# Optimization experiments

Hardware: AMD Instinct MI355X
Metric: run time of the kernel (lower is better)

## Reference

```python
import jax, jax.numpy as jnp
import numpy as np

NQ = 4  # qubits
silu = jax.nn.silu


def _ry(t):
    c, s = jnp.cos(t / 2), jnp.sin(t / 2)
    return jnp.stack([jnp.stack([c, -s]), jnp.stack([s, c])]).astype(jnp.complex64)


def _rz(t):
    e = jnp.exp(-0.5j * t.astype(jnp.complex64))
    z = jnp.zeros((), jnp.complex64)
    return jnp.stack([jnp.stack([e, z]), jnp.stack([z, jnp.conj(e)])])


def _ap1(state, U, w):
    # apply 2x2 unitary U on wire w of a (2,)*NQ statevector
    s = jnp.tensordot(U, jnp.moveaxis(state, w, 0), axes=1)
    return jnp.moveaxis(s, 0, w)


def _cnot(state, c, t):
    s = jnp.moveaxis(state, (c, t), (0, 1))
    s = jnp.stack([s[0], s[1, ::-1]], axis=0)
    return jnp.moveaxis(s, (0, 1), (c, t))


def _circuit(inp, w):
    # batched 4-qubit state-vector simulation of the PennyLane qnode
    state = jnp.zeros((2,) * NQ, jnp.complex64).at[(0,) * NQ].set(1.0)
    for i in range(NQ):
        state = _ap1(state, _ry(inp[i]), i)
    for i in range(NQ):
        state = _ap1(state, _rz(w[i, 0]), i)
        state = _ap1(state, _ry(w[i, 1]), i)
    for i in range(NQ - 1):
        state = _cnot(state, i, i + 1)
    for i in range(NQ):
        state = _ap1(state, _rz(w[i + NQ, 0]), i)
        state = _ap1(state, _ry(w[i + NQ, 1]), i)
    p = state.real ** 2 + state.imag ** 2
    sign = jnp.array([1.0, -1.0], p.dtype)
    return jnp.stack([jnp.tensordot(p, sign, axes=[[i], [0]]).sum() for i in range(NQ)])


def _bn(x, p, eps=1e-5):
    # p: [4, C] = (gamma, beta, running_mean, running_var); eval-mode batchnorm
    g, b, m, v = p
    shp = (1, -1) + (1,) * (x.ndim - 2)
    return (x - m.reshape(shp)) * (g.reshape(shp) / jnp.sqrt(v.reshape(shp) + eps)) + b.reshape(shp)


def _conv(x, w, b, pad, dil=1):
    y = jax.lax.conv_general_dilated(x, w, (1,), [(pad, pad)], rhs_dilation=(dil,),
                                     dimension_numbers=('NCH', 'OIH', 'NCH'))
    return y + b[None, :, None]


def _forward(x, W1, b1, bn1, Wa1, ba1, bna1, Wa2, ba2, bna2,
             Wd1, bd1, bnd1, Wd2, bd2, bnd2, Wr1, br1, bnr1, Wr2, br2, bnr2,
             Wfm, bfm, qw, Wf1, bf1, bnf1, Wf2, bf2, bnf2, Wf3, bf3):
    h = silu(_bn(_conv(x, W1, b1, 2), bn1))                    # [B,64,L]
    a = silu(_bn(_conv(h, Wa1, ba1, 3), bna1))                 # [B,32,L]
    a = jax.nn.sigmoid(_bn(_conv(a, Wa2, ba2, 3), bna2))       # [B,64,L]
    h = h * a
    h = silu(_bn(_conv(h, Wd1, bd1, 2, 2), bnd1))              # [B,128,L]
    h = silu(_bn(_conv(h, Wd2, bd2, 4, 4), bnd2))              # [B,128,L]
    idn = h
    r = silu(_bn(_conv(h, Wr1, br1, 1), bnr1))
    r = _bn(_conv(r, Wr2, br2, 1), bnr2)                       # (dropout is identity in eval)
    h = silu(r + idn)
    g = h.mean(axis=2)                                         # global avg pool -> [B,128]
    qin = g @ Wfm.T + bfm                                      # feature map -> [B,4]
    q = jax.vmap(_circuit, in_axes=(0, None))(qin, qw)         # [B,4]
    x1 = silu(_bn(q @ Wf1.T + bf1, bnf1))
    x2 = silu(_bn(x1 @ Wf2.T + bf2, bnf2))
    return x2 @ Wf3.T + bf3                                    # [B,1]


def setup_inputs() -> dict:
    key = jax.random.key(0)
    ks = iter(jax.random.split(key, 64))

    def w(*shape, scale=0.05):
        return jax.random.normal(next(ks), shape, jnp.float32) * scale

    def bnp(c):
        g = 1.0 + 0.1 * jax.random.normal(next(ks), (c,), jnp.float32)
        b = 0.1 * jax.random.normal(next(ks), (c,), jnp.float32)
        m = 0.1 * jax.random.normal(next(ks), (c,), jnp.float32)
        v = 1.0 + 0.1 * jax.random.uniform(next(ks), (c,), jnp.float32)
        return jnp.stack([g, b, m, v])

    B, L = 128, 4096
    return dict(
        x=jax.random.normal(next(ks), (B, 1, L), jnp.float32),
        W1=w(64, 1, 5), b1=w(64), bn1=bnp(64),
        Wa1=w(32, 64, 7), ba1=w(32), bna1=bnp(32),
        Wa2=w(64, 32, 7), ba2=w(64), bna2=bnp(64),
        Wd1=w(128, 64, 3), bd1=w(128), bnd1=bnp(128),
        Wd2=w(128, 128, 3), bd2=w(128), bnd2=bnp(128),
        Wr1=w(128, 128, 3), br1=w(128), bnr1=bnp(128),
        Wr2=w(128, 128, 3), br2=w(128), bnr2=bnp(128),
        Wfm=w(4, 128), bfm=w(4),
        qw=jax.random.uniform(next(ks), (8, 2), jnp.float32, 0.0, 2 * np.pi),
        Wf1=w(64, 4, scale=0.2), bf1=w(64), bnf1=bnp(64),
        Wf2=w(32, 64, scale=0.2), bf2=w(32), bnf2=bnp(32),
        Wf3=w(1, 32, scale=0.2), bf3=w(1),
    )


def reference(x, W1, b1, bn1, Wa1, ba1, bna1, Wa2, ba2, bna2,
              Wd1, bd1, bnd1, Wd2, bd2, bnd2, Wr1, br1, bnr1, Wr2, br2, bnr2,
              Wfm, bfm, qw, Wf1, bf1, bnf1, Wf2, bf2, bnf2, Wf3, bf3):
    return _forward(x, W1, b1, bn1, Wa1, ba1, bna1, Wa2, ba2, bna2,
                    Wd1, bd1, bnd1, Wd2, bd2, bnd2, Wr1, br1, bnr1, Wr2, br2, bnr2,
                    Wfm, bfm, qw, Wf1, bf1, bnf1, Wf2, bf2, bnf2, Wf3, bf3)
```

## Files before the change

kernel.cpp:

```cpp
#include <hip/hip_runtime.h>
#include <math.h>

#define L_LEN 4096
#define DEV __device__ __forceinline__

typedef __attribute__((ext_vector_type(8))) _Float16 f16x8;
typedef __attribute__((ext_vector_type(4))) float   f32x4;

DEV float fexp_f(float x) { return exp2f(1.44269504f * x); }
DEV float silu_f(float x) { return x * __builtin_amdgcn_rcpf(1.f + fexp_f(-x)); }
DEV float sigm_f(float x) { return __builtin_amdgcn_rcpf(1.f + fexp_f(-x)); }

DEV void gload16(const void* g, void* l) {
    __builtin_amdgcn_global_load_lds(
        (const __attribute__((address_space(1))) void*)g,
        (__attribute__((address_space(3))) void*)l, 16, 0, 0);
}

__global__ __launch_bounds__(256) void conv1_k(
    const float* __restrict__ x, const float* __restrict__ W,
    const float* __restrict__ bias, const float* __restrict__ bnp,
    _Float16* __restrict__ out)
{
    __shared__ float sw[64 * 5];
    __shared__ float ssc[64], ssh[64];
    const int tid = threadIdx.x;
    if (tid < 64) {
        float g = bnp[tid], be = bnp[64 + tid], mn = bnp[128 + tid], vr = bnp[192 + tid];
        float sc = g * rsqrtf(vr + 1e-5f);
        ssc[tid] = sc;
        ssh[tid] = fmaf(bias[tid] - mn, sc, be);
    }
    for (int i = tid; i < 320; i += 256) sw[i] = W[i];
    __syncthreads();

    const int b = blockIdx.y;
    const int l = blockIdx.x * 64 + (tid >> 2);
    const int cq = (tid & 3) * 16;

    float win[5];
#pragma unroll
    for (int k = 0; k < 5; ++k) {
        int ix = l + k - 2;
        win[k] = (ix >= 0 && ix < L_LEN) ? x[(size_t)b * L_LEN + ix] : 0.f;
    }
    __align__(16) _Float16 vv[16];
#pragma unroll
    for (int j = 0; j < 16; ++j) {
        const int co = cq + j;
        float z = 0.f;
#pragma unroll
        for (int k = 0; k < 5; ++k) z = fmaf(sw[co * 5 + k], win[k], z);
        z = fmaf(z, ssc[co], ssh[co]);
        vv[j] = (_Float16)silu_f(z);
    }
    const size_t o = ((size_t)b * L_LEN + l) * 64 + cq;
    *(int4*)(out + o)     = *(const int4*)(vv);
    *(int4*)(out + o + 8) = *(const int4*)(vv + 8);
}

struct PrepArgs {
    const float* W[6];
    _Float16*    wf[6];
    int cin[6], cout[6], kk[6];
    int cum[7];
};

__global__ void prep_all_k(PrepArgs a)
{
    const int id0 = blockIdx.x * 256 + threadIdx.x;
    if (id0 >= a.cum[6]) return;
    int sg = 0;
    while (sg < 5 && id0 >= a.cum[sg + 1]) ++sg;
    const int id   = id0 - a.cum[sg];
    const int CIN  = a.cin[sg], COUT = a.cout[sg], K = a.kk[sg];
    const int NTILE = COUT / 16;
    const int lane = id & 63;
    int r = id >> 6;
    const int n = r % NTILE; r /= NTILE;
    const int t = r % K;
    const int s = r / K;

    const int co  = n * 16 + (lane & 15);
    const int cib = s * 32 + (lane >> 4) * 8;
    const float* W = a.W[sg];
    __align__(16) _Float16 v8[8];
#pragma unroll
    for (int j = 0; j < 8; ++j)
        v8[j] = (_Float16)W[((size_t)co * CIN + cib + j) * K + t];
    *(int4*)(a.wf[sg] + (size_t)id * 8) = *(const int4*)v8;
}

template <int CIN, int COUT, int K, int DIL, int MODE>
__launch_bounds__(256, 2) __global__ void conv_mfma_k(
    const _Float16* __restrict__ in, const _Float16* __restrict__ wf,
    const float* __restrict__ bias,  const float* __restrict__ bnp,
    const _Float16* __restrict__ aux, _Float16* __restrict__ out,
    float* __restrict__ gsum, const float* __restrict__ zpage)
{
    constexpr int SL    = CIN / 32;
    constexpr int P     = SL * K;
    constexpr int PADR  = ((K - 1) / 2) * DIL;
    constexpr int LWIN  = 128 + (K - 1) * DIL;
    constexpr int NT    = COUT / 32;
    constexpr int NTILE = COUT / 16;
    constexpr int SLOTS = CIN / 8 + 1;
    constexpr int RSTR  = SLOTS * 16;
    constexpr int CH_IN = LWIN * SLOTS;
    constexpr int STGB  = LWIN * RSTR;
    constexpr int ESTR  = COUT + 4;
    constexpr int EPIB  = 128 * ESTR * 2;
    constexpr int SMEMB = (MODE == 3) ? STGB : ((STGB > EPIB) ? STGB : EPIB);

    __shared__ __align__(16) char smem[SMEMB];
    __shared__ float pf[(MODE == 3) ? 2 : 1][COUT];

    const int tid   = threadIdx.x;
    const int lane  = tid & 63;
    const int w     = tid >> 6;
    const int wl    = w >> 1;
    const int wc    = w & 1;
    const int b     = blockIdx.z;
    const int l0    = blockIdx.x * 128;
    const int lan15 = lane & 15;
    const int kgB   = (lane >> 4) * 16;

    const size_t bL = (size_t)b * L_LEN;

    auto loadB = [&](int p, f16x8 (&dst)[NT]) {
        const _Float16* bbase = wf + (size_t)p * (NTILE * 512);
#pragma unroll
        for (int nt = 0; nt < NT; ++nt) {
            const int ntg = wc * NT + nt;
            dst[nt] = *(const f16x8*)(bbase + ntg * 512 + lane * 8);
        }
    };

    f32x4 acc[4][NT];
#pragma unroll
    for (int mt = 0; mt < 4; ++mt)
#pragma unroll
        for (int nt = 0; nt < NT; ++nt) acc[mt][nt] = (f32x4){0.f, 0.f, 0.f, 0.f};

    f16x8 brbuf[2][NT];

    for (int c = tid; c < CH_IN; c += 256) {
        const int row  = c / SLOTS;
        const int slot = c - row * SLOTS;
        const int gl   = l0 - PADR + row;
        const bool ok  = (slot < SLOTS - 1) & (gl >= 0) & (gl < L_LEN);
        const _Float16* s0 = in + ((bL + gl) * CIN + slot * 8);
        const void* src = ok ? (const void*)s0 : (const void*)zpage;
        gload16(src, smem + (size_t)c * 16);
    }
    loadB(0, brbuf[0]);
    if (P > 1) loadB(1, brbuf[1]);
    asm volatile("s_waitcnt vmcnt(0)" ::: "memory");
    __builtin_amdgcn_sched_barrier(0);
    __syncthreads();

#pragma unroll
    for (int pp = 0; pp < P; ++pp) {
        const int ss = pp / K;
        const int tt = pp % K;
#pragma unroll
        for (int mt = 0; mt < 4; ++mt) {
            const int row = wl * 64 + mt * 16 + lan15 + tt * DIL;
            const f16x8 a = *(const f16x8*)(smem + row * RSTR + ss * 64 + kgB);
#pragma unroll
            for (int nt = 0; nt < NT; ++nt) {
                acc[mt][nt] = __builtin_amdgcn_mfma_f32_16x16x32_f16(brbuf[pp & 1][nt], a, acc[mt][nt], 0, 0, 0);
            }
        }
        if (pp + 2 < P) loadB(pp + 2, brbuf[pp & 1]);
    }

    if constexpr (MODE == 3) {
#pragma unroll
        for (int nt = 0; nt < NT; ++nt) {
            const int co0 = (wc * NT + nt) * 16 + (lane >> 4) * 4;
            const float4 g4 = *(const float4*)&bnp[co0];
            const float4 b4 = *(const float4*)&bnp[COUT + co0];
            const float4 m4 = *(const float4*)&bnp[2 * COUT + co0];
            const float4 v4 = *(const float4*)&bnp[3 * COUT + co0];
            const float4 bi = *(const float4*)&bias[co0];
            float sc[4], sh[4];
            sc[0] = g4.x * rsqrtf(v4.x + 1e-5f); sh[0] = fmaf(bi.x - m4.x, sc[0], b4.x);
            sc[1] = g4.y * rsqrtf(v4.y + 1e-5f); sh[1] = fmaf(bi.y - m4.y, sc[1], b4.y);
            sc[2] = g4.z * rsqrtf(v4.z + 1e-5f); sh[2] = fmaf(bi.z - m4.z, sc[2], b4.z);
            sc[3] = g4.w * rsqrtf(v4.w + 1e-5f); sh[3] = fmaf(bi.w - m4.w, sc[3], b4.w);

            float ps[4] = {0.f, 0.f, 0.f, 0.f};
#pragma unroll
            for (int mt = 0; mt < 4; ++mt) {
                const int l = wl * 64 + mt * 16 + lan15;
                const size_t gi = (bL + l0 + l) * COUT + co0;
                _Float16 a4[4];
                *(int2*)a4 = *(const int2*)(aux + gi);
#pragma unroll
                for (int r = 0; r < 4; ++r)
                    ps[r] += silu_f(fmaf(acc[mt][nt][r], sc[r], sh[r]) + (float)a4[r]);
            }
#pragma unroll
            for (int r = 0; r < 4; ++r) {
                ps[r] += __shfl_xor(ps[r], 1, 64);
                ps[r] += __shfl_xor(ps[r], 2, 64);
                ps[r] += __shfl_xor(ps[r], 4, 64);
                ps[r] += __shfl_xor(ps[r], 8, 64);
            }
            if (lan15 == 0) {
#pragma unroll
                for (int r = 0; r < 4; ++r)
                    pf[wl][co0 + r] = ps[r];
            }
        }
        __syncthreads();
        if (tid < COUT)
            atomicAdd(&gsum[b * COUT + tid], pf[0][tid] + pf[1][tid]);
    } else {
        __syncthreads();
        _Float16* zl = (_Float16*)smem;
#pragma unroll
        for (int nt = 0; nt < NT; ++nt) {
            const int co0 = (wc * NT + nt) * 16 + (lane >> 4) * 4;
            const float4 g4 = *(const float4*)&bnp[co0];
            const float4 b4 = *(const float4*)&bnp[COUT + co0];
            const float4 m4 = *(const float4*)&bnp[2 * COUT + co0];
            const float4 v4 = *(const float4*)&bnp[3 * COUT + co0];
            const float4 bi = *(const float4*)&bias[co0];
            float sc[4], sh[4];
            sc[0] = g4.x * rsqrtf(v4.x + 1e-5f); sh[0] = fmaf(bi.x - m4.x, sc[0], b4.x);
            sc[1] = g4.y * rsqrtf(v4.y + 1e-5f); sh[1] = fmaf(bi.y - m4.y, sc[1], b4.y);
            sc[2] = g4.z * rsqrtf(v4.z + 1e-5f); sh[2] = fmaf(bi.z - m4.z, sc[2], b4.z);
            sc[3] = g4.w * rsqrtf(v4.w + 1e-5f); sh[3] = fmaf(bi.w - m4.w, sc[3], b4.w);
#pragma unroll
            for (int mt = 0; mt < 4; ++mt) {
                const int l_loc = wl * 64 + mt * 16 + lan15;
                __align__(8) _Float16 h4[4];
#pragma unroll
                for (int r = 0; r < 4; ++r)
                    h4[r] = (_Float16)fmaf(acc[mt][nt][r], sc[r], sh[r]);
                *(int2*)&zl[l_loc * ESTR + co0] = *(const int2*)h4;
            }
        }
        __syncthreads();

        constexpr int CO8 = COUT / 8;
        constexpr int LG  = (CO8 == 16) ? 4 : (CO8 == 8) ? 3 : 2;
        constexpr int RPI = 64 / CO8;
        const int co = (lane & (CO8 - 1)) * 8;

#pragma unroll
        for (int s2 = 0; s2 < CO8 / 2; ++s2) {
            const int l = w * 32 + s2 * RPI + (lane >> LG);
            _Float16 z8[8];
            *(int4*)z8 = *(const int4*)&zl[l * ESTR + co];
            const size_t gidx = (bL + l0 + l) * COUT + co;
            __align__(16) _Float16 o8[8];
            if constexpr (MODE == 0) {
#pragma unroll
                for (int j = 0; j < 8; ++j) o8[j] = (_Float16)silu_f((float)z8[j]);
            } else {
                _Float16 g8[8];
                *(int4*)g8 = *(const int4*)(aux + gidx);
#pragma unroll
                for (int j = 0; j < 8; ++j) o8[j] = (_Float16)((float)g8[j] * sigm_f((float)z8[j]));
            }
            *(int4*)(out + gidx) = *(const int4*)o8;
        }
    }
}

template <int BW> DEV void g_ry(float (&re)[16], float (&im)[16], float t) {
    float s, c; sincosf(0.5f * t, &s, &c);
#pragma unroll
    for (int i = 0; i < 16; ++i)
        if (!(i & BW)) {
            const int j = i | BW;
            float r0 = re[i], q0 = im[i], r1 = re[j], q1 = im[j];
            re[i] = c * r0 - s * r1; im[i] = c * q0 - s * q1;
            re[j] = s * r0 + c * r1; im[j] = s * q0 + c * q1;
        }
}
template <int BW> DEV void g_rz(float (&re)[16], float (&im)[16], float t) {
    float s, c; sincosf(0.5f * t, &s, &c);
#pragma unroll
    for (int i = 0; i < 16; ++i) {
        float r = re[i], q = im[i];
        if (i & BW) { re[i] = r * c - q * s; im[i] = q * c + r * s; }
        else        { re[i] = r * c + q * s; im[i] = q * c - r * s; }
    }
}
template <int BC, int BT> DEV void g_cnot(float (&re)[16], float (&im)[16]) {
#pragma unroll
    for (int i = 0; i < 16; ++i)
        if ((i & BC) && !(i & BT)) {
            const int j = i | BT;
            float r = re[i]; re[i] = re[j]; re[j] = r;
            float q = im[i]; im[i] = im[j]; im[j] = q;
        }
}

__global__ __launch_bounds__(64) void qhead_k(
    const float* __restrict__ gsum, const float* __restrict__ Wfm,
    const float* __restrict__ bfm, const float* __restrict__ qw,
    const float* __restrict__ Wf1, const float* __restrict__ bf1, const float* __restrict__ bnf1,
    const float* __restrict__ Wf2, const float* __restrict__ bf2, const float* __restrict__ bnf2,
    const float* __restrict__ Wf3, const float* __restrict__ bf3,
    float* __restrict__ out)
{
    const int b = blockIdx.x, t = threadIdx.x;
    const float inv = 1.f / (float)L_LEN;

    float part[4];
    {
        const float gv0 = gsum[b * 128 + t] * inv;
        const float gv1 = gsum[b * 128 + 64 + t] * inv;
#pragma unroll
        for (int j = 0; j < 4; ++j)
            part[j] = gv0 * Wfm[j * 128 + t] + gv1 * Wfm[j * 128 + 64 + t];
    }
#pragma unroll
    for (int j = 0; j < 4; ++j) {
#pragma unroll
        for (int m = 1; m < 64; m <<= 1)
            part[j] += __shfl_xor(part[j], m, 64);
        part[j] += bfm[j];
    }

    float re[16], im[16];
#pragma unroll
    for (int i = 0; i < 16; ++i) { re[i] = 0.f; im[i] = 0.f; }
    re[0] = 1.f;
    g_ry<8>(re, im, part[0]); g_ry<4>(re, im, part[1]); g_ry<2>(re, im, part[2]); g_ry<1>(re, im, part[3]);
    g_rz<8>(re, im, qw[0]);  g_ry<8>(re, im, qw[1]);
    g_rz<4>(re, im, qw[2]);  g_ry<4>(re, im, qw[3]);
    g_rz<2>(re, im, qw[4]);  g_ry<2>(re, im, qw[5]);
    g_rz<1>(re, im, qw[6]);  g_ry<1>(re, im, qw[7]);
    g_cnot<8, 4>(re, im); g_cnot<4, 2>(re, im); g_cnot<2, 1>(re, im);
    g_rz<8>(re, im, qw[8]);  g_ry<8>(re, im, qw[9]);
    g_rz<4>(re, im, qw[10]); g_ry<4>(re, im, qw[11]);
    g_rz<2>(re, im, qw[12]); g_ry<2>(re, im, qw[13]);
    g_rz<1>(re, im, qw[14]); g_ry<1>(re, im, qw[15]);

    float pr[16];
#pragma unroll
    for (int i = 0; i < 16; ++i) pr[i] = re[i] * re[i] + im[i] * im[i];
    float q[4];
#pragma unroll
    for (int w = 0; w < 4; ++w) {
        const int bw = 8 >> w;
        float e = 0.f;
#pragma unroll
        for (int i = 0; i < 16; ++i) e += (i & bw) ? -pr[i] : pr[i];
        q[w] = e;
    }

    __shared__ float x1[64], x2[32];
    {
        float a = bf1[t];
#pragma unroll
        for (int k = 0; k < 4; ++k) a = fmaf(q[k], Wf1[t * 4 + k], a);
        const float sc = bnf1[t] / sqrtf(bnf1[192 + t] + 1e-5f);
        const float z  = (a - bnf1[128 + t]) * sc + bnf1[64 + t];
        x1[t] = silu_f(z);
    }
    __syncthreads();
    if (t < 32) {
        float a = bf2[t];
        for (int k = 0; k < 64; ++k) a = fmaf(x1[k], Wf2[t * 64 + k], a);
        const float sc = bnf2[t] / sqrtf(bnf2[96 + t] + 1e-5f);
        const float z  = (a - bnf2[64 + t]) * sc + bnf2[32 + t];
        x2[t] = silu_f(z);
    }
    __syncthreads();
    if (t == 0) {
        float a = bf3[0];
        for (int k = 0; k < 32; ++k) a = fmaf(x2[k], Wf3[k], a);
        out[b] = a;
    }
}

extern "C" void kernel_launch(void* const* d_in, const int* in_sizes, int n_in,
                              void* d_out, int out_size, void* d_ws, size_t ws_size,
                              hipStream_t stream)
{
    (void)n_in; (void)out_size;
    const float* x    = (const float*)d_in[0];
    const float* W1   = (const float*)d_in[1];
    const float* b1   = (const float*)d_in[2];
    const float* bn1  = (const float*)d_in[3];
    const float* Wa1  = (const float*)d_in[4];
    const float* ba1  = (const float*)d_in[5];
    const float* bna1 = (const float*)d_in[6];
    const float* Wa2  = (const float*)d_in[7];
    const float* ba2  = (const float*)d_in[8];
    const float* bna2 = (const float*)d_in[9];
    const float* Wd1  = (const float*)d_in[10];
    const float* bdd1 = (const float*)d_in[11];
    const float* bnd1 = (const float*)d_in[12];
    const float* Wd2  = (const float*)d_in[13];
    const float* bdd2 = (const float*)d_in[14];
    const float* bnd2 = (const float*)d_in[15];
    const float* Wr1  = (const float*)d_in[16];
    const float* br1  = (const float*)d_in[17];
    const float* bnr1 = (const float*)d_in[18];
    const float* Wr2  = (const float*)d_in[19];
    const float* br2  = (const float*)d_in[20];
    const float* bnr2 = (const float*)d_in[21];
    const float* Wfm  = (const float*)d_in[22];
    const float* bfm  = (const float*)d_in[23];
    const float* qw   = (const float*)d_in[24];
    const float* Wf1  = (const float*)d_in[25];
    const float* bf1  = (const float*)d_in[26];
    const float* bnf1 = (const float*)d_in[27];
    const float* Wf2  = (const float*)d_in[28];
    const float* bf2  = (const float*)d_in[29];
    const float* bnf2 = (const float*)d_in[30];
    const float* Wf3  = (const float*)d_in[31];
    const float* bf3  = (const float*)d_in[32];

    const int B = in_sizes[0] / L_LEN;

    char* base = (char*)d_ws;
    size_t off = 0;
    auto alloc = [&](size_t bytes) -> char* {
        off = (off + 255) & ~(size_t)255;
        char* p = base + off;
        off += bytes;
        return p;
    };

    float* gbuf  = (float*)alloc((size_t)B * 128 * 4);
    float* zpage = (float*)alloc(256);

    auto wfrag = [&](int cin, int cout, int k) -> _Float16* {
        return (_Float16*)alloc((size_t)k * cout * cin * 2);
    };
    _Float16* wa1f = wfrag(64, 32, 7);
    _Float16* wa2f = wfrag(32, 64, 7);
    _Float16* wd1f = wfrag(64, 128, 3);
    _Float16* wd2f = wfrag(128, 128, 3);
    _Float16* wr1f = wfrag(128, 128, 3);
    _Float16* wr2f = wfrag(128, 128, 3);

    const size_t fixed = (off + 255) & ~(size_t)255;
    const size_t PS = (size_t)2 * L_LEN * 256;
    size_t avail = (ws_size > fixed + 4096) ? ws_size - fixed - 4096 : 0;
    int chunk = B;
    while (chunk > 1 && (size_t)chunk * PS > avail) chunk >>= 1;

    auto aplane = [&](int C, int c) -> _Float16* {
        return (_Float16*)alloc((size_t)c * L_LEN * C * 2);
    };
    _Float16* h0 = aplane(64,  chunk);
    _Float16* a1 = aplane(32,  chunk);
    (void)     aplane(32,  chunk);
    _Float16* d1 = aplane(128, chunk);
    _Float16* d2 = h0;
    _Float16* r1 = d1;

    PrepArgs pa;
    pa.W[0] = Wa1; pa.wf[0] = wa1f; pa.cin[0] = 64;  pa.cout[0] = 32;  pa.kk[0] = 7;
    pa.W[1] = Wa2; pa.wf[1] = wa2f; pa.cin[1] = 32;  pa.cout[1] = 64;  pa.kk[1] = 7;
    pa.W[2] = Wd1; pa.wf[2] = wd1f; pa.cin[2] = 64;  pa.cout[2] = 128; pa.kk[2] = 3;
    pa.W[3] = Wd2; pa.wf[3] = wd2f; pa.cin[3] = 128; pa.cout[3] = 128; pa.kk[3] = 3;
    pa.W[4] = Wr1; pa.wf[4] = wr1f; pa.cin[4] = 128; pa.cout[4] = 128; pa.kk[4] = 3;
    pa.W[5] = Wr2; pa.wf[5] = wr2f; pa.cin[5] = 128; pa.cout[5] = 128; pa.kk[5] = 3;
    pa.cum[0] = 0;
    for (int i = 0; i < 6; ++i)
        pa.cum[i + 1] = pa.cum[i] + (pa.cin[i] / 32) * pa.kk[i] * (pa.cout[i] / 16) * 64;
    prep_all_k<<<dim3((pa.cum[6] + 255) / 256), dim3(256), 0, stream>>>(pa);

    hipMemsetAsync(gbuf, 0, (size_t)B * 128 * sizeof(float), stream);
    hipMemsetAsync(zpage, 0, 256, stream);

    const dim3 blk(256);
    for (int sft = 0; sft < B; sft += chunk) {
        const int c = (chunk < B - sft) ? chunk : (B - sft);
        const dim3 cg(L_LEN / 128, 1, c);
        conv1_k<<<dim3(64, c), blk, 0, stream>>>(x + (size_t)sft * L_LEN, W1, b1, bn1, h0);
        conv_mfma_k<64, 32, 7, 1, 0><<<cg, blk, 0, stream>>>(h0, wa1f, ba1, bna1, nullptr, a1, nullptr, zpage);
        conv_mfma_k<32, 64, 7, 1, 1><<<cg, blk, 0, stream>>>(a1, wa2f, ba2, bna2, h0, h0, nullptr, zpage);
        conv_mfma_k<64, 128, 3, 2, 0><<<cg, blk, 0, stream>>>(h0, wd1f, bdd1, bnd1, nullptr, d1, nullptr, zpage);
        conv_mfma_k<128, 128, 3, 4, 0><<<cg, blk, 0, stream>>>(d1, wd2f, bdd2, bnd2, nullptr, d2, nullptr, zpage);
        conv_mfma_k<128, 128, 3, 1, 0><<<cg, blk, 0, stream>>>(d2, wr1f, br1, bnr1, nullptr, r1, nullptr, zpage);
        conv_mfma_k<128, 128, 3, 1, 3><<<cg, blk, 0, stream>>>(r1, wr2f, br2, bnr2, d2, nullptr, gbuf + (size_t)sft * 128, zpage);
    }

    qhead_k<<<dim3(B), dim3(64), 0, stream>>>(gbuf, Wfm, bfm, qw,
                                              Wf1, bf1, bnf1, Wf2, bf2, bnf2, Wf3, bf3,
                                              (float*)d_out);
}
```

Measured before the change: 454.1 us.

## Process two L-tiles per block with double-buffered input staging

```diff
diff --git a/kernel.cpp b/kernel.cpp
--- a/kernel.cpp
+++ b/kernel.cpp
@@ -98,6 +98,7 @@
     const _Float16* __restrict__ aux, _Float16* __restrict__ out,
     float* __restrict__ gsum, const float* __restrict__ zpage)
 {
+    constexpr int TT    = 2;
     constexpr int SL    = CIN / 32;
     constexpr int P     = SL * K;
     constexpr int PADR  = ((K - 1) / 2) * DIL;
@@ -107,10 +108,12 @@
     constexpr int SLOTS = CIN / 8 + 1;
     constexpr int RSTR  = SLOTS * 16;
     constexpr int CH_IN = LWIN * SLOTS;
-    constexpr int STGB  = LWIN * RSTR;
+    constexpr int BUFB  = LWIN * RSTR;
     constexpr int ESTR  = COUT + 4;
     constexpr int EPIB  = 128 * ESTR * 2;
-    constexpr int SMEMB = (MODE == 3) ? STGB : ((STGB > EPIB) ? STGB : EPIB);
+    constexpr bool EFIT = (EPIB <= BUFB);
+    constexpr int SMEMB = (MODE == 3) ? 2 * BUFB
+                        : (EFIT ? 2 * BUFB : 2 * BUFB + EPIB);
 
     __shared__ __align__(16) char smem[SMEMB];
     __shared__ float pf[(MODE == 3) ? 2 : 1][COUT];
@@ -121,11 +124,24 @@
     const int wl    = w >> 1;
     const int wc    = w & 1;
     const int b     = blockIdx.z;
-    const int l0    = blockIdx.x * 128;
     const int lan15 = lane & 15;
     const int kgB   = (lane >> 4) * 16;
+    const int tile0 = blockIdx.x * TT;
 
     const size_t bL = (size_t)b * L_LEN;
+
+    auto stage_in = [&](int l0s, int buf) {
+        char* dst = smem + buf * BUFB;
+        for (int c = tid; c < CH_IN; c += 256) {
+            const int row  = c / SLOTS;
+            const int slot = c - row * SLOTS;
+            const int gl   = l0s - PADR + row;
+            const bool ok  = (slot < SLOTS - 1) & (gl >= 0) & (gl < L_LEN);
+            const _Float16* s0 = in + ((bL + gl) * CIN + slot * 8);
+            const void* src = ok ? (const void*)s0 : (const void*)zpage;
+            gload16(src, dst + (size_t)c * 16);
+        }
+    };
 
     auto loadB = [&](int p, f16x8 (&dst)[NT]) {
         const _Float16* bbase = wf + (size_t)p * (NTILE * 512);
@@ -136,137 +152,154 @@
         }
     };
 
-    f32x4 acc[4][NT];
-#pragma unroll
-    for (int mt = 0; mt < 4; ++mt)
-#pragma unroll
-        for (int nt = 0; nt < NT; ++nt) acc[mt][nt] = (f32x4){0.f, 0.f, 0.f, 0.f};
-
-    f16x8 brbuf[2][NT];
-
-    for (int c = tid; c < CH_IN; c += 256) {
-        const int row  = c / SLOTS;
-        const int slot = c - row * SLOTS;
-        const int gl   = l0 - PADR + row;
-        const bool ok  = (slot < SLOTS - 1) & (gl >= 0) & (gl < L_LEN);
-        const _Float16* s0 = in + ((bL + gl) * CIN + slot * 8);
-        const void* src = ok ? (const void*)s0 : (const void*)zpage;
-        gload16(src, smem + (size_t)c * 16);
-    }
-    loadB(0, brbuf[0]);
-    if (P > 1) loadB(1, brbuf[1]);
-    asm volatile("s_waitcnt vmcnt(0)" ::: "memory");
-    __builtin_amdgcn_sched_barrier(0);
-    __syncthreads();
-
-#pragma unroll
-    for (int pp = 0; pp < P; ++pp) {
-        const int ss = pp / K;
-        const int tt = pp % K;
-#pragma unroll
-        for (int mt = 0; mt < 4; ++mt) {
-            const int row = wl * 64 + mt * 16 + lan15 + tt * DIL;
-            const f16x8 a = *(const f16x8*)(smem + row * RSTR + ss * 64 + kgB);
+    stage_in(tile0 * 128, 0);
+
+#pragma unroll
+    for (int ti = 0; ti < TT; ++ti) {
+        const int l0  = (tile0 + ti) * 128;
+        char* curb = smem + (ti & 1) * BUFB;
+
+        asm volatile("s_waitcnt vmcnt(0)" ::: "memory");
+        __builtin_amdgcn_sched_barrier(0);
+        __syncthreads();
+
+        f32x4 acc[4][NT];
+#pragma unroll
+        for (int mt = 0; mt < 4; ++mt)
+#pragma unroll
+            for (int nt = 0; nt < NT; ++nt) acc[mt][nt] = (f32x4){0.f, 0.f, 0.f, 0.f};
+
+        f16x8 brbuf[2][NT];
+        loadB(0, brbuf[0]);
+        if (P > 1) loadB(1, brbuf[1]);
+
+#pragma unroll
+        for (int pp = 0; pp < P; ++pp) {
+            const int ss = pp / K;
+            const int tt = pp % K;
+#pragma unroll
+            for (int mt = 0; mt < 4; ++mt) {
+                const int row = wl * 64 + mt * 16 + lan15 + tt * DIL;
+                const f16x8 a = *(const f16x8*)(curb + row * RSTR + ss * 64 + kgB);
+#pragma unroll
+                for (int nt = 0; nt < NT; ++nt)
+                    acc[mt][nt] = __builtin_amdgcn_mfma_f32_16x16x32_f16(brbuf[pp & 1][nt], a, acc[mt][nt], 0, 0, 0);
+            }
+            if (pp + 2 < P) loadB(pp + 2, brbuf[pp & 1]);
+        }
+
+        if constexpr (MODE == 3) {
+            int2 a16[4][NT];
+#pragma unroll
+            for (int mt = 0; mt < 4; ++mt)
+#pragma unroll
+                for (int nt = 0; nt < NT; ++nt) {
+                    const int co0 = (wc * NT + nt) * 16 + (lane >> 4) * 4;
+                    const int l = wl * 64 + mt * 16 + lan15;
+                    a16[mt][nt] = *(const int2*)(aux + (bL + l0 + l) * COUT + co0);
+                }
+            if (ti + 1 < TT) stage_in(l0 + 128, (ti + 1) & 1);
+
 #pragma unroll
             for (int nt = 0; nt < NT; ++nt) {
-                acc[mt][nt] = __builtin_amdgcn_mfma_f32_16x16x32_f16(brbuf[pp & 1][nt], a, acc[mt][nt], 0, 0, 0);
+                const int co0 = (wc * NT + nt) * 16 + (lane >> 4) * 4;
+                const float4 g4 = *(const float4*)&bnp[co0];
+                const float4 b4 = *(const float4*)&bnp[COUT + co0];
+                const float4 m4 = *(const float4*)&bnp[2 * COUT + co0];
+                const float4 v4 = *(const float4*)&bnp[3 * COUT + co0];
+                const float4 bi = *(const float4*)&bias[co0];
+                float sc[4], sh[4];
+                sc[0] = g4.x * rsqrtf(v4.x + 1e-5f); sh[0] = fmaf(bi.x - m4.x, sc[0], b4.x);
+                sc[1] = g4.y * rsqrtf(v4.y + 1e-5f); sh[1] = fmaf(bi.y - m4.y, sc[1], b4.y);
+                sc[2] = g4.z * rsqrtf(v4.z + 1e-5f); sh[2] = fmaf(bi.z - m4.z, sc[2], b4.z);
+                sc[3] = g4.w * rsqrtf(v4.w + 1e-5f); sh[3] = fmaf(bi.w - m4.w, sc[3], b4.w);
+
+                float ps[4] = {0.f, 0.f, 0.f, 0.f};
+#pragma unroll
+                for (int mt = 0; mt < 4; ++mt) {
+                    _Float16 a4[4];
+                    *(int2*)a4 = a16[mt][nt];
+#pragma unroll
+                    for (int r = 0; r < 4; ++r)
+                        ps[r] += silu_f(fmaf(acc[mt][nt][r], sc[r], sh[r]) + (float)a4[r]);
+                }
+#pragma unroll
+                for (int r = 0; r < 4; ++r) {
+                    ps[r] += __shfl_xor(ps[r], 1, 64);
+                    ps[r] += __shfl_xor(ps[r], 2, 64);
+                    ps[r] += __shfl_xor(ps[r], 4, 64);
+                    ps[r] += __shfl_xor(ps[r], 8, 64);
+                }
+                if (lan15 == 0) {
+#pragma unroll
+                    for (int r = 0; r < 4; ++r)
+                        pf[wl][co0 + r] = ps[r];
+                }
             }
-        }
-        if (pp + 2 < P) loadB(pp + 2, brbuf[pp & 1]);
-    }
-
-    if constexpr (MODE == 3) {
-#pragma unroll
-        for (int nt = 0; nt < NT; ++nt) {
-            const int co0 = (wc * NT + nt) * 16 + (lane >> 4) * 4;
-            const float4 g4 = *(const float4*)&bnp[co0];
-            const float4 b4 = *(const float4*)&bnp[COUT + co0];
-            const float4 m4 = *(const float4*)&bnp[2 * COUT + co0];
-            const float4 v4 = *(const float4*)&bnp[3 * COUT + co0];
-            const float4 bi = *(const float4*)&bias[co0];
-            float sc[4], sh[4];
-            sc[0] = g4.x * rsqrtf(v4.x + 1e-5f); sh[0] = fmaf(bi.x - m4.x, sc[0], b4.x);
-            sc[1] = g4.y * rsqrtf(v4.y + 1e-5f); sh[1] = fmaf(bi.y - m4.y, sc[1], b4.y);
-            sc[2] = g4.z * rsqrtf(v4.z + 1e-5f); sh[2] = fmaf(bi.z - m4.z, sc[2], b4.z);
-            sc[3] = g4.w * rsqrtf(v4.w + 1e-5f); sh[3] = fmaf(bi.w - m4.w, sc[3], b4.w);
-
-            float ps[4] = {0.f, 0.f, 0.f, 0.f};
-#pragma unroll
-            for (int mt = 0; mt < 4; ++mt) {
-                const int l = wl * 64 + mt * 16 + lan15;
-                const size_t gi = (bL + l0 + l) * COUT + co0;
-                _Float16 a4[4];
-                *(int2*)a4 = *(const int2*)(aux + gi);
-#pragma unroll
-                for (int r = 0; r < 4; ++r)
-                    ps[r] += silu_f(fmaf(acc[mt][nt][r], sc[r], sh[r]) + (float)a4[r]);
+            __syncthreads();
+            if (tid < COUT)
+                atomicAdd(&gsum[b * COUT + tid], pf[0][tid] + pf[1][tid]);
+        } else {
+            constexpr int CO8 = COUT / 8;
+            constexpr int LG  = (CO8 == 16) ? 4 : (CO8 == 8) ? 3 : 2;
+            constexpr int RPI = 64 / CO8;
+            const int cos = (lane & (CO8 - 1)) * 8;
+
+            int4 gx[CO8 / 2];
+            if constexpr (MODE == 1) {
+#pragma unroll
+                for (int s2 = 0; s2 < CO8 / 2; ++s2) {
+                    const int l = w * 32 + s2 * RPI + (lane >> LG);
+                    gx[s2] = *(const int4*)(aux + (bL + l0 + l) * COUT + cos);
+                }
             }
-#pragma unroll
-            for (int r = 0; r < 4; ++r) {
-                ps[r] += __shfl_xor(ps[r], 1, 64);
-                ps[r] += __shfl_xor(ps[r], 2, 64);
-                ps[r] += __shfl_xor(ps[r], 4, 64);
-                ps[r] += __shfl_xor(ps[r], 8, 64);
+            if (ti + 1 < TT) stage_in(l0 + 128, (ti + 1) & 1);
+
+            __syncthreads();
+            _Float16* zl = EFIT ? (_Float16*)curb : (_Float16*)(smem + 2 * BUFB);
+#pragma unroll
+            for (int nt = 0; nt < NT; ++nt) {
+                const int co0 = (wc * NT + nt) * 16 + (lane >> 4) * 4;
+                const float4 g4 = *(const float4*)&bnp[co0];
+                const float4 b4 = *(const float4*)&bnp[COUT + co0];
+                const float4 m4 = *(const float4*)&bnp[2 * COUT + co0];
+                const float4 v4 = *(const float4*)&bnp[3 * COUT + co0];
+                const float4 bi = *(const float4*)&bias[co0];
+                float sc[4], sh[4];
+                sc[0] = g4.x * rsqrtf(v4.x + 1e-5f); sh[0] = fmaf(bi.x - m4.x, sc[0], b4.x);
+                sc[1] = g4.y * rsqrtf(v4.y + 1e-5f); sh[1] = fmaf(bi.y - m4.y, sc[1], b4.y);
+                sc[2] = g4.z * rsqrtf(v4.z + 1e-5f); sh[2] = fmaf(bi.z - m4.z, sc[2], b4.z);
+                sc[3] = g4.w * rsqrtf(v4.w + 1e-5f); sh[3] = fmaf(bi.w - m4.w, sc[3], b4.w);
+#pragma unroll
+                for (int mt = 0; mt < 4; ++mt) {
+                    const int l_loc = wl * 64 + mt * 16 + lan15;
+                    __align__(8) _Float16 h4[4];
+#pragma unroll
+                    for (int r = 0; r < 4; ++r)
+                        h4[r] = (_Float16)fmaf(acc[mt][nt][r], sc[r], sh[r]);
+                    *(int2*)&zl[l_loc * ESTR + co0] = *(const int2*)h4;
+                }
             }
-            if (lan15 == 0) {
-#pragma unroll
-                for (int r = 0; r < 4; ++r)
-                    pf[wl][co0 + r] = ps[r];
+            __syncthreads();
+
+#pragma unroll
+            for (int s2 = 0; s2 < CO8 / 2; ++s2) {
+                const int l = w * 32 + s2 * RPI + (lane >> LG);
+                _Float16 z8[8];
+                *(int4*)z8 = *(const int4*)&zl[l * ESTR + cos];
+                const size_t gidx = (bL + l0 + l) * COUT + cos;
+                __align__(16) _Float16 o8[8];
+                if constexpr (MODE == 0) {
+#pragma unroll
+                    for (int j = 0; j < 8; ++j) o8[j] = (_Float16)silu_f((float)z8[j]);
+                } else {
+                    _Float16 g8[8];
+                    *(int4*)g8 = gx[s2];
+#pragma unroll
+                    for (int j = 0; j < 8; ++j) o8[j] = (_Float16)((float)g8[j] * sigm_f((float)z8[j]));
+                }
+                *(int4*)(out + gidx) = *(const int4*)o8;
             }
-        }
-        __syncthreads();
-        if (tid < COUT)
-            atomicAdd(&gsum[b * COUT + tid], pf[0][tid] + pf[1][tid]);
-    } else {
-        __syncthreads();
-        _Float16* zl = (_Float16*)smem;
-#pragma unroll
-        for (int nt = 0; nt < NT; ++nt) {
-            const int co0 = (wc * NT + nt) * 16 + (lane >> 4) * 4;
-            const float4 g4 = *(const float4*)&bnp[co0];
-            const float4 b4 = *(const float4*)&bnp[COUT + co0];
-            const float4 m4 = *(const float4*)&bnp[2 * COUT + co0];
-            const float4 v4 = *(const float4*)&bnp[3 * COUT + co0];
-            const float4 bi = *(const float4*)&bias[co0];
-            float sc[4], sh[4];
-            sc[0] = g4.x * rsqrtf(v4.x + 1e-5f); sh[0] = fmaf(bi.x - m4.x, sc[0], b4.x);
-            sc[1] = g4.y * rsqrtf(v4.y + 1e-5f); sh[1] = fmaf(bi.y - m4.y, sc[1], b4.y);
-            sc[2] = g4.z * rsqrtf(v4.z + 1e-5f); sh[2] = fmaf(bi.z - m4.z, sc[2], b4.z);
-            sc[3] = g4.w * rsqrtf(v4.w + 1e-5f); sh[3] = fmaf(bi.w - m4.w, sc[3], b4.w);
-#pragma unroll
-            for (int mt = 0; mt < 4; ++mt) {
-                const int l_loc = wl * 64 + mt * 16 + lan15;
-                __align__(8) _Float16 h4[4];
-#pragma unroll
-                for (int r = 0; r < 4; ++r)
-                    h4[r] = (_Float16)fmaf(acc[mt][nt][r], sc[r], sh[r]);
-                *(int2*)&zl[l_loc * ESTR + co0] = *(const int2*)h4;
-            }
-        }
-        __syncthreads();
-
-        constexpr int CO8 = COUT / 8;
-        constexpr int LG  = (CO8 == 16) ? 4 : (CO8 == 8) ? 3 : 2;
-        constexpr int RPI = 64 / CO8;
-        const int co = (lane & (CO8 - 1)) * 8;
-
-#pragma unroll
-        for (int s2 = 0; s2 < CO8 / 2; ++s2) {
-            const int l = w * 32 + s2 * RPI + (lane >> LG);
-            _Float16 z8[8];
-            *(int4*)z8 = *(const int4*)&zl[l * ESTR + co];
-            const size_t gidx = (bL + l0 + l) * COUT + co;
-            __align__(16) _Float16 o8[8];
-            if constexpr (MODE == 0) {
-#pragma unroll
-                for (int j = 0; j < 8; ++j) o8[j] = (_Float16)silu_f((float)z8[j]);
-            } else {
-                _Float16 g8[8];
-                *(int4*)g8 = *(const int4*)(aux + gidx);
-#pragma unroll
-                for (int j = 0; j < 8; ++j) o8[j] = (_Float16)((float)g8[j] * sigm_f((float)z8[j]));
-            }
-            *(int4*)(out + gidx) = *(const int4*)o8;
         }
     }
 }
@@ -478,7 +511,7 @@
     const dim3 blk(256);
     for (int sft = 0; sft < B; sft += chunk) {
         const int c = (chunk < B - sft) ? chunk : (B - sft);
-        const dim3 cg(L_LEN / 128, 1, c);
+        const dim3 cg(L_LEN / 256, 1, c);
         conv1_k<<<dim3(64, c), blk, 0, stream>>>(x + (size_t)sft * L_LEN, W1, b1, bn1, h0);
         conv_mfma_k<64, 32, 7, 1, 0><<<cg, blk, 0, stream>>>(h0, wa1f, ba1, bna1, nullptr, a1, nullptr, zpage);
         conv_mfma_k<32, 64, 7, 1, 1><<<cg, blk, 0, stream>>>(a1, wa2f, ba2, bna2, h0, h0, nullptr, zpage);
```

New measurement: 502.0 us. 1.11x slower.
